# Performance work log

Measured on AMD Instinct MI355X. Metric: run time of the kernel, lower is better.

The kernel has to match this reference:

```python
import jax, jax.numpy as jnp
import numpy as np

H = 256; L = 4; NH = 8; S = 2; N = 1024; E = 32768


def _ln(x, g, b, eps=1e-5):
    m = x.mean(-1, keepdims=True)
    v = x.var(-1, keepdims=True)
    return (x - m) / jnp.sqrt(v + eps) * g + b


def _mha(h, in_w, in_b, out_w, out_b):
    # torch nn.MultiheadAttention (batch_first): h [B, T, H]
    B, T, Hd = h.shape
    qkv = h @ in_w.T + in_b  # [B, T, 3H]
    q, k, v = jnp.split(qkv, 3, axis=-1)
    d = Hd // NH
    def rs(a):
        return a.reshape(B, T, NH, d).transpose(0, 2, 1, 3)  # [B, nh, T, d]
    q, k, v = rs(q), rs(k), rs(v)
    att = jax.nn.softmax(jnp.einsum('bhqd,bhkd->bhqk', q, k) * (1.0 / np.sqrt(d)), axis=-1)
    o = jnp.einsum('bhqk,bhkd->bhqd', att, v).transpose(0, 2, 1, 3).reshape(B, T, Hd)
    return o @ out_w.T + out_b


def _forward(edge_index, x, fe_w1, fe_b1, fe_w2, fe_b2,
             g_inw, g_inb, g_outw, g_outb, g_m1w, g_m1b, g_m2w, g_m2b,
             g_n1g, g_n1b, g_n2g, g_n2b,
             t_inw, t_inb, t_outw, t_outb, t_l1w, t_l1b, t_l2w, t_l2b,
             t_n1g, t_n1b, t_n2g, t_n2b, o_w1, o_b1, o_w2, o_b2):
    row, col = edge_index[0], edge_index[1]
    # feature encoder: [S, N, 3] -> [S, N, H]
    h = jnp.maximum(x @ fe_w1.T + fe_b1, 0.0) @ fe_w2.T + fe_b2
    # construct_graph uses first 3 channels of encoded features as positions
    pos = h[..., :3]
    ea = pos[:, col] - pos[:, row]  # [S, E, 3] edge_attr, fixed across GNN layers
    cnt = jnp.maximum(jax.ops.segment_sum(jnp.ones((E,), h.dtype), row, num_segments=N), 1.0)
    for l in range(L):
        hn = _ln(h, g_n1g[l], g_n1b[l])
        a = _mha(hn, g_inw[l], g_inb[l], g_outw[l], g_outb[l]) + h  # dense attn over N nodes, S as batch
        ef = jnp.concatenate([a[:, col], ea], axis=-1)  # gather: [S, E, H+3]
        msg = jnp.maximum(ef @ g_m1w[l].T + g_m1b[l], 0.0) @ g_m2w[l].T + g_m2b[l]  # [S, E, H]
        agg = jax.vmap(lambda m: jax.ops.segment_sum(m, row, num_segments=N))(msg)  # scatter-sum
        agg = agg / cnt[None, :, None]  # scatter-mean
        h = _ln(agg, g_n2g[l], g_n2b[l]) + h
    # temporal transformer over S per node: [N, S, H] (B=1 so B*N = N)
    ht = h.transpose(1, 0, 2)
    for l in range(L):
        a = _mha(ht, t_inw[l], t_inb[l], t_outw[l], t_outb[l])
        ht = _ln(ht + a, t_n1g[l], t_n1b[l])  # post-norm TransformerEncoderLayer, relu FFN
        ff = jnp.maximum(ht @ t_l1w[l].T + t_l1b[l], 0.0) @ t_l2w[l].T + t_l2b[l]
        ht = _ln(ht + ff, t_n2g[l], t_n2b[l])
    last = ht[:, -1, :]  # [N, H]
    out = jnp.maximum(last @ o_w1.T + o_b1, 0.0) @ o_w2.T + o_b2  # [N, 3]
    # reshape(B,N,out_seq,-1).transpose(1,2).squeeze(0) with B=1, out_seq=1 -> [1, N, 3]
    return out.reshape(1, N, 3)


def setup_inputs():
    key = jax.random.key(0)
    ks = iter(jax.random.split(key, 40))
    def w(shape, s=0.02):
        return jax.random.normal(next(ks), shape, dtype=jnp.float32) * s
    inp = {}
    inp['x'] = jax.random.normal(next(ks), (S, N, 3), dtype=jnp.float32)
    inp['edge_index'] = jax.random.randint(next(ks), (2, E), 0, N, dtype=jnp.int32)
    inp['fe_w1'] = w((H, 3)); inp['fe_b1'] = jnp.zeros((H,), jnp.float32)
    inp['fe_w2'] = w((H, H)); inp['fe_b2'] = jnp.zeros((H,), jnp.float32)
    inp['g_inw'] = w((L, 3 * H, H)); inp['g_inb'] = jnp.zeros((L, 3 * H), jnp.float32)
    inp['g_outw'] = w((L, H, H)); inp['g_outb'] = jnp.zeros((L, H), jnp.float32)
    inp['g_m1w'] = w((L, H, H + 3)); inp['g_m1b'] = jnp.zeros((L, H), jnp.float32)
    inp['g_m2w'] = w((L, H, H)); inp['g_m2b'] = jnp.zeros((L, H), jnp.float32)
    inp['g_n1g'] = jnp.ones((L, H), jnp.float32); inp['g_n1b'] = jnp.zeros((L, H), jnp.float32)
    inp['g_n2g'] = jnp.ones((L, H), jnp.float32); inp['g_n2b'] = jnp.zeros((L, H), jnp.float32)
    inp['t_inw'] = w((L, 3 * H, H)); inp['t_inb'] = jnp.zeros((L, 3 * H), jnp.float32)
    inp['t_outw'] = w((L, H, H)); inp['t_outb'] = jnp.zeros((L, H), jnp.float32)
    inp['t_l1w'] = w((L, 4 * H, H)); inp['t_l1b'] = jnp.zeros((L, 4 * H), jnp.float32)
    inp['t_l2w'] = w((L, H, 4 * H)); inp['t_l2b'] = jnp.zeros((L, H), jnp.float32)
    inp['t_n1g'] = jnp.ones((L, H), jnp.float32); inp['t_n1b'] = jnp.zeros((L, H), jnp.float32)
    inp['t_n2g'] = jnp.ones((L, H), jnp.float32); inp['t_n2b'] = jnp.zeros((L, H), jnp.float32)
    inp['o_w1'] = w((H, H)); inp['o_b1'] = jnp.zeros((H,), jnp.float32)
    inp['o_w2'] = w((3, H)); inp['o_b2'] = jnp.zeros((3,), jnp.float32)
    return inp


def reference(x, edge_index, fe_w1, fe_b1, fe_w2, fe_b2,
              g_inw, g_inb, g_outw, g_outb, g_m1w, g_m1b, g_m2w, g_m2b,
              g_n1g, g_n1b, g_n2g, g_n2b,
              t_inw, t_inb, t_outw, t_outb, t_l1w, t_l1b, t_l2w, t_l2b,
              t_n1g, t_n1b, t_n2g, t_n2b, o_w1, o_b1, o_w2, o_b2):
    return _forward(edge_index, x, fe_w1, fe_b1, fe_w2, fe_b2,
                    g_inw, g_inb, g_outw, g_outb, g_m1w, g_m1b, g_m2w, g_m2b,
                    g_n1g, g_n1b, g_n2g, g_n2b,
                    t_inw, t_inb, t_outw, t_outb, t_l1w, t_l1b, t_l2w, t_l2b,
                    t_n1g, t_n1b, t_n2g, t_n2b, o_w1, o_b1, o_w2, o_b2)
```

## Files before the change

### kernel.cpp

```cpp
#include <hip/hip_runtime.h>
#include <math.h>

#define NN 1024
#define SS 2
#define HH 256
#define EE 32768
#define NHEAD 8
#define LL 4

template<bool RELU, bool RESID, bool ROWSCALE>
__global__ __launch_bounds__(256)
void gemm_xwt32(const float* __restrict__ X, int ldx,
                const float* __restrict__ W, int ldw,
                const float* __restrict__ bias,
                const float* __restrict__ resid, int ldr,
                const float* __restrict__ rowscale,
                float* __restrict__ Y, int ldy, int K)
{
    __shared__ __align__(16) float Xs[16][68];
    __shared__ __align__(16) float Ws[16][36];
    const int tid = threadIdx.x;
    const int bn0 = blockIdx.x * 32;
    const int bm0 = blockIdx.y * 64;
    const int tx = tid & 7, ty = tid >> 3;
    const int lc = tid & 15, lr = tid >> 4;
    float acc[2][4];
#pragma unroll
    for (int i = 0; i < 2; i++)
#pragma unroll
        for (int j = 0; j < 4; j++) acc[i][j] = 0.f;

    for (int k0 = 0; k0 < K; k0 += 16) {
#pragma unroll
        for (int i = 0; i < 4; i++) {
            int r = lr * 4 + i;
            Xs[lc][r] = X[(size_t)(bm0 + r) * ldx + k0 + lc];
        }
#pragma unroll
        for (int i = 0; i < 2; i++) {
            int r = lr * 2 + i;
            Ws[lc][r] = W[(size_t)(bn0 + r) * ldw + k0 + lc];
        }
        __syncthreads();
#pragma unroll
        for (int kk = 0; kk < 16; kk++) {
            float2 av = *reinterpret_cast<const float2*>(&Xs[kk][ty * 2]);
            float4 bv = *reinterpret_cast<const float4*>(&Ws[kk][tx * 4]);
            float a2[2] = {av.x, av.y};
            float b4[4] = {bv.x, bv.y, bv.z, bv.w};
#pragma unroll
            for (int i = 0; i < 2; i++)
#pragma unroll
                for (int j = 0; j < 4; j++)
                    acc[i][j] = fmaf(a2[i], b4[j], acc[i][j]);
        }
        __syncthreads();
    }
#pragma unroll
    for (int i = 0; i < 2; i++) {
        int m = bm0 + ty * 2 + i;
        float rs = ROWSCALE ? rowscale[m] : 1.f;
        float* yp = Y + (size_t)m * ldy + bn0 + tx * 4;
        const float* rp = RESID ? (resid + (size_t)m * ldr + bn0 + tx * 4) : nullptr;
#pragma unroll
        for (int j = 0; j < 4; j++) {
            float b = bias[bn0 + tx * 4 + j];
            float v = acc[i][j] + (ROWSCALE ? rs * b : b);
            if (RESID) v += rp[j];
            if (RELU) v = fmaxf(v, 0.f);
            yp[j] = v;
        }
    }
}

template<bool RESID>
__global__ __launch_bounds__(256)
void ln_kernel(const float* __restrict__ X, const float* __restrict__ g,
               const float* __restrict__ b, const float* __restrict__ resid,
               float* __restrict__ Y)
{
    int row = blockIdx.x, t = threadIdx.x;
    float v = X[(size_t)row * HH + t];
    float s1 = v, s2 = v * v;
#pragma unroll
    for (int m = 32; m >= 1; m >>= 1) {
        s1 += __shfl_xor(s1, m);
        s2 += __shfl_xor(s2, m);
    }
    __shared__ float w1[4], w2[4];
    if ((t & 63) == 0) { w1[t >> 6] = s1; w2[t >> 6] = s2; }
    __syncthreads();
    float tot1 = w1[0] + w1[1] + w1[2] + w1[3];
    float tot2 = w2[0] + w2[1] + w2[2] + w2[3];
    float mean = tot1 * (1.f / HH);
    float var = tot2 * (1.f / HH) - mean * mean;
    float inv = rsqrtf(var + 1e-5f);
    float out = (v - mean) * inv * g[t] + b[t];
    if (RESID) out += resid[(size_t)row * HH + t];
    Y[(size_t)row * HH + t] = out;
}

__global__ __launch_bounds__(256, 2)
void attn_graph_kernel(const float* __restrict__ qkv, float* __restrict__ out)
{
    const int s = blockIdx.z, hh = blockIdx.y, qt = blockIdx.x;
    const int tid = threadIdx.x;
    const int qslot = tid >> 4, sub = tid & 15;
    __shared__ __align__(16) float Qs[32][36];
    __shared__ __align__(16) float Ks[128][36];
    __shared__ __align__(16) float Vs[128][36];
    const float* base = qkv + (size_t)s * NN * 768;
    {
        int r = tid >> 3, c0 = (tid & 7) * 4;
        const float* src = base + (size_t)(qt * 32 + r) * 768 + hh * 32 + c0;
        *reinterpret_cast<float4*>(&Qs[r][c0]) = *reinterpret_cast<const float4*>(src);
    }
    __syncthreads();
    float qa[32], qb[32], oa[32], ob[32];
#pragma unroll
    for (int c = 0; c < 32; c++) {
        qa[c] = Qs[qslot * 2][c];
        qb[c] = Qs[qslot * 2 + 1][c];
        oa[c] = 0.f; ob[c] = 0.f;
    }
    float ma = -INFINITY, la = 0.f;
    float mb = -INFINITY, lb = 0.f;
    const float scale = 0.17677669529663687f;

    for (int kc = 0; kc < NN; kc += 128) {
        __syncthreads();
        {
            int r0 = tid >> 3, c0 = (tid & 7) * 4;
#pragma unroll
            for (int u = 0; u < 4; u++) {
                int r = r0 + 32 * u;
                const float* ksrc = base + (size_t)(kc + r) * 768 + 256 + hh * 32 + c0;
                *reinterpret_cast<float4*>(&Ks[r][c0]) = *reinterpret_cast<const float4*>(ksrc);
                *reinterpret_cast<float4*>(&Vs[r][c0]) = *reinterpret_cast<const float4*>(ksrc + 256);
            }
        }
        __syncthreads();
        float sa[8], sb[8];
#pragma unroll
        for (int i = 0; i < 8; i++) {
            int j = sub + 16 * i;
            float da = 0.f, db = 0.f;
#pragma unroll
            for (int c = 0; c < 32; c++) {
                float kv = Ks[j][c];
                da = fmaf(qa[c], kv, da);
                db = fmaf(qb[c], kv, db);
            }
            sa[i] = da * scale;
            sb[i] = db * scale;
        }
        float cma = sa[0], cmb = sb[0];
#pragma unroll
        for (int i = 1; i < 8; i++) { cma = fmaxf(cma, sa[i]); cmb = fmaxf(cmb, sb[i]); }
        float mna = fmaxf(ma, cma), mnb = fmaxf(mb, cmb);
        float ca = __expf(ma - mna), cb = __expf(mb - mnb);
        la *= ca; lb *= cb;
#pragma unroll
        for (int c = 0; c < 32; c++) { oa[c] *= ca; ob[c] *= cb; }
#pragma unroll
        for (int i = 0; i < 8; i++) {
            int j = sub + 16 * i;
            float pa = __expf(sa[i] - mna);
            float pb = __expf(sb[i] - mnb);
            la += pa; lb += pb;
#pragma unroll
            for (int c = 0; c < 32; c++) {
                float vv = Vs[j][c];
                oa[c] = fmaf(pa, vv, oa[c]);
                ob[c] = fmaf(pb, vv, ob[c]);
            }
        }
        ma = mna; mb = mnb;
    }
#pragma unroll
    for (int mask = 1; mask <= 8; mask <<= 1) {
        float m2a = __shfl_xor(ma, mask), l2a = __shfl_xor(la, mask);
        float mna = fmaxf(ma, m2a);
        float c1a = __expf(ma - mna), c2a = __expf(m2a - mna);
        la = la * c1a + l2a * c2a;
        float m2b = __shfl_xor(mb, mask), l2b = __shfl_xor(lb, mask);
        float mnb = fmaxf(mb, m2b);
        float c1b = __expf(mb - mnb), c2b = __expf(m2b - mnb);
        lb = lb * c1b + l2b * c2b;
#pragma unroll
        for (int c = 0; c < 32; c++) {
            float ta = __shfl_xor(oa[c], mask);
            oa[c] = oa[c] * c1a + ta * c2a;
            float tb = __shfl_xor(ob[c], mask);
            ob[c] = ob[c] * c1b + tb * c2b;
        }
        ma = mna; mb = mnb;
    }
    float ia = 1.f / la, ib = 1.f / lb;
    float* dA = out + ((size_t)s * NN + qt * 32 + qslot * 2) * HH + hh * 32;
    float* dB = dA + HH;
#pragma unroll
    for (int c2 = 0; c2 < 16; c2++) {
        if (c2 == sub) {
            *reinterpret_cast<float2*>(dA + c2 * 2) =
                make_float2(oa[c2 * 2] * ia, oa[c2 * 2 + 1] * ia);
            *reinterpret_cast<float2*>(dB + c2 * 2) =
                make_float2(ob[c2 * 2] * ib, ob[c2 * 2 + 1] * ib);
        }
    }
}

__global__ __launch_bounds__(256)
void attn_t2_kernel(const float* __restrict__ qkvt, float* __restrict__ out)
{
    int idx = blockIdx.x * 256 + threadIdx.x;
    int n = idx >> 3, hh = idx & 7;
    const float* p0 = qkvt + ((size_t)n * SS + 0) * 768 + hh * 32;
    const float* p1 = qkvt + ((size_t)n * SS + 1) * 768 + hh * 32;
    float s00 = 0, s01 = 0, s10 = 0, s11 = 0;
#pragma unroll
    for (int c4 = 0; c4 < 8; c4++) {
        float4 q0 = *reinterpret_cast<const float4*>(p0 + c4 * 4);
        float4 q1 = *reinterpret_cast<const float4*>(p1 + c4 * 4);
        float4 k0 = *reinterpret_cast<const float4*>(p0 + 256 + c4 * 4);
        float4 k1 = *reinterpret_cast<const float4*>(p1 + 256 + c4 * 4);
        s00 += q0.x * k0.x + q0.y * k0.y + q0.z * k0.z + q0.w * k0.w;
        s01 += q0.x * k1.x + q0.y * k1.y + q0.z * k1.z + q0.w * k1.w;
        s10 += q1.x * k0.x + q1.y * k0.y + q1.z * k0.z + q1.w * k0.w;
        s11 += q1.x * k1.x + q1.y * k1.y + q1.z * k1.z + q1.w * k1.w;
    }
    const float scale = 0.17677669529663687f;
    s00 *= scale; s01 *= scale; s10 *= scale; s11 *= scale;
    float m0 = fmaxf(s00, s01), m1 = fmaxf(s10, s11);
    float p00 = __expf(s00 - m0), p01 = __expf(s01 - m0);
    float p10 = __expf(s10 - m1), p11 = __expf(s11 - m1);
    float i0 = 1.f / (p00 + p01), i1 = 1.f / (p10 + p11);
    p00 *= i0; p01 *= i0; p10 *= i1; p11 *= i1;
    float* o0 = out + ((size_t)n * SS + 0) * HH + hh * 32;
    float* o1 = out + ((size_t)n * SS + 1) * HH + hh * 32;
#pragma unroll
    for (int c4 = 0; c4 < 8; c4++) {
        float4 v0 = *reinterpret_cast<const float4*>(p0 + 512 + c4 * 4);
        float4 v1 = *reinterpret_cast<const float4*>(p1 + 512 + c4 * 4);
        float4 r0, r1;
        r0.x = p00 * v0.x + p01 * v1.x; r0.y = p00 * v0.y + p01 * v1.y;
        r0.z = p00 * v0.z + p01 * v1.z; r0.w = p00 * v0.w + p01 * v1.w;
        r1.x = p10 * v0.x + p11 * v1.x; r1.y = p10 * v0.y + p11 * v1.y;
        r1.z = p10 * v0.z + p11 * v1.z; r1.w = p10 * v0.w + p11 * v1.w;
        *reinterpret_cast<float4*>(o0 + c4 * 4) = r0;
        *reinterpret_cast<float4*>(o1 + c4 * 4) = r1;
    }
}

__global__ __launch_bounds__(256)
void edge_agg_kernel(const float* __restrict__ P, const float* __restrict__ ea,
                     const float* __restrict__ W1,
                     const int* __restrict__ off, const int* __restrict__ eid,
                     const int* __restrict__ colIdx, const float* __restrict__ cnt,
                     float* __restrict__ Rn)
{
    const int n = blockIdx.x, s = blockIdx.y;
    const int t = threadIdx.x;
    const float w0 = W1[(size_t)t * 259 + 256];
    const float w1 = W1[(size_t)t * 259 + 257];
    const float w2 = W1[(size_t)t * 259 + 258];
    float acc = 0.f;
    const int beg = off[n], end = off[n + 1];
    const float* eab = ea + (size_t)s * EE * 3;
    const float* Pb = P + (size_t)s * NN * HH;
    for (int p = beg; p < end; ++p) {
        int e = eid[p];
        int c = colIdx[e];
        float e0 = eab[(size_t)e * 3 + 0];
        float e1 = eab[(size_t)e * 3 + 1];
        float e2 = eab[(size_t)e * 3 + 2];
        float u = Pb[(size_t)c * HH + t] + e0 * w0 + e1 * w1 + e2 * w2;
        acc += fmaxf(u, 0.f);
    }
    Rn[((size_t)s * NN + n) * HH + t] = acc / cnt[n];
}

__global__ __launch_bounds__(256)
void enc1_kernel(const float* __restrict__ x, const float* __restrict__ w1,
                 const float* __restrict__ b1, float* __restrict__ t0)
{
    int m = blockIdx.x, j = threadIdx.x;
    float x0 = x[(size_t)m * 3 + 0], x1 = x[(size_t)m * 3 + 1], x2 = x[(size_t)m * 3 + 2];
    float v = fmaf(x0, w1[j * 3 + 0], fmaf(x1, w1[j * 3 + 1], fmaf(x2, w1[j * 3 + 2], b1[j])));
    t0[(size_t)m * HH + j] = fmaxf(v, 0.f);
}

__global__ __launch_bounds__(256)
void deg_kernel(const int* __restrict__ rowIdx, int* __restrict__ deg)
{
    int e = blockIdx.x * 256 + threadIdx.x;
    atomicAdd(&deg[rowIdx[e]], 1);
}

__global__ __launch_bounds__(256)
void cnt_kernel(const int* __restrict__ deg, float* __restrict__ cnt,
                float* __restrict__ bscale)
{
    int n = blockIdx.x * 256 + threadIdx.x;
    int d = deg[n];
    cnt[n] = d > 0 ? (float)d : 1.f;
    float bs = d > 0 ? 1.f : 0.f;
    bscale[n] = bs;
    bscale[NN + n] = bs;
}

__global__ void scan1024(const int* __restrict__ deg, int* __restrict__ off)
{
    __shared__ int tmp[1024];
    int t = threadIdx.x;
    tmp[t] = deg[t];
    __syncthreads();
    for (int d = 1; d < 1024; d <<= 1) {
        int v = 0;
        if (t >= d) v = tmp[t - d];
        __syncthreads();
        if (t >= d) tmp[t] += v;
        __syncthreads();
    }
    off[t + 1] = tmp[t];
    if (t == 0) off[0] = 0;
}

__global__ __launch_bounds__(256)
void csr_scatter(const int* __restrict__ rowIdx, int* __restrict__ cursor,
                 int* __restrict__ eidb)
{
    int e = blockIdx.x * 256 + threadIdx.x;
    int p = atomicAdd(&cursor[rowIdx[e]], 1);
    eidb[p] = e;
}

__global__ __launch_bounds__(256)
void ea_kernel(const float* __restrict__ h, const int* __restrict__ rowIdx,
               const int* __restrict__ colIdx, float* __restrict__ ea)
{
    int idx = blockIdx.x * 256 + threadIdx.x;
    int e = idx & (EE - 1);
    int s = idx >> 15;
    int r = rowIdx[e], c = colIdx[e];
    const float* hb = h + (size_t)s * NN * HH;
    float* o = ea + (size_t)idx * 3;
    o[0] = hb[(size_t)c * HH + 0] - hb[(size_t)r * HH + 0];
    o[1] = hb[(size_t)c * HH + 1] - hb[(size_t)r * HH + 1];
    o[2] = hb[(size_t)c * HH + 2] - hb[(size_t)r * HH + 2];
}

__global__ __launch_bounds__(256)
void transpose_sn(const float* __restrict__ h, float* __restrict__ ht)
{
    int c = threadIdx.x, n = blockIdx.x, s = blockIdx.y;
    ht[((size_t)n * SS + s) * HH + c] = h[((size_t)s * NN + n) * HH + c];
}

__global__ __launch_bounds__(64)
void final_kernel(const float* __restrict__ o1, const float* __restrict__ w2,
                  const float* __restrict__ b2, float* __restrict__ out)
{
    int n = blockIdx.x, t = threadIdx.x;
    float a0 = 0, a1 = 0, a2 = 0;
#pragma unroll
    for (int r = 0; r < 4; r++) {
        float v = o1[(size_t)n * HH + t + 64 * r];
        a0 = fmaf(v, w2[0 * HH + t + 64 * r], a0);
        a1 = fmaf(v, w2[1 * HH + t + 64 * r], a1);
        a2 = fmaf(v, w2[2 * HH + t + 64 * r], a2);
    }
#pragma unroll
    for (int m = 32; m >= 1; m >>= 1) {
        a0 += __shfl_xor(a0, m);
        a1 += __shfl_xor(a1, m);
        a2 += __shfl_xor(a2, m);
    }
    if (t == 0) {
        out[(size_t)n * 3 + 0] = a0 + b2[0];
        out[(size_t)n * 3 + 1] = a1 + b2[1];
        out[(size_t)n * 3 + 2] = a2 + b2[2];
    }
}

extern "C" void kernel_launch(void* const* d_in, const int* in_sizes, int n_in,
                              void* d_out, int out_size, void* d_ws, size_t ws_size,
                              hipStream_t stream)
{
    const float* x      = (const float*)d_in[0];
    const int*   eidx   = (const int*)d_in[1];
    const float* fe_w1  = (const float*)d_in[2];
    const float* fe_b1  = (const float*)d_in[3];
    const float* fe_w2  = (const float*)d_in[4];
    const float* fe_b2  = (const float*)d_in[5];
    const float* g_inw  = (const float*)d_in[6];
    const float* g_inb  = (const float*)d_in[7];
    const float* g_outw = (const float*)d_in[8];
    const float* g_outb = (const float*)d_in[9];
    const float* g_m1w  = (const float*)d_in[10];
    const float* g_m1b  = (const float*)d_in[11];
    const float* g_m2w  = (const float*)d_in[12];
    const float* g_m2b  = (const float*)d_in[13];
    const float* g_n1g  = (const float*)d_in[14];
    const float* g_n1b  = (const float*)d_in[15];
    const float* g_n2g  = (const float*)d_in[16];
    const float* g_n2b  = (const float*)d_in[17];
    const float* t_inw  = (const float*)d_in[18];
    const float* t_inb  = (const float*)d_in[19];
    const float* t_outw = (const float*)d_in[20];
    const float* t_outb = (const float*)d_in[21];
    const float* t_l1w  = (const float*)d_in[22];
    const float* t_l1b  = (const float*)d_in[23];
    const float* t_l2w  = (const float*)d_in[24];
    const float* t_l2b  = (const float*)d_in[25];
    const float* t_n1g  = (const float*)d_in[26];
    const float* t_n1b  = (const float*)d_in[27];
    const float* t_n2g  = (const float*)d_in[28];
    const float* t_n2b  = (const float*)d_in[29];
    const float* o_w1   = (const float*)d_in[30];
    const float* o_b1   = (const float*)d_in[31];
    const float* o_w2   = (const float*)d_in[32];
    const float* o_b2   = (const float*)d_in[33];

    const int* rowIdx = eidx;
    const int* colIdx = eidx + EE;

    float* w = (float*)d_ws;
    const size_t F = (size_t)SS * NN * HH;
    float* h      = w;
    float* hn     = w + F;
    float* qkv    = w + 2 * F;
    float* attno  = w + 5 * F;
    float* a      = w + 6 * F;
    float* P      = w + 7 * F;
    float* Rn     = w + 8 * F;
    float* aggn   = w + 9 * F;
    float* ffh    = w + 10 * F;
    float* ea     = w + 14 * F;
    float* o1     = ea + (size_t)SS * EE * 3;
    float* cnt    = o1 + (size_t)NN * HH;
    float* bscale = cnt + NN;
    int* ib       = (int*)(bscale + 2 * NN);
    int* deg      = ib;
    int* off      = ib + NN;
    int* cursor   = ib + 2 * NN + 1;
    int* eidbuf   = ib + 3 * NN + 1;

    dim3 b256(256);

    float* t0 = qkv;
    enc1_kernel<<<dim3(SS * NN), b256, 0, stream>>>(x, fe_w1, fe_b1, t0);
    gemm_xwt32<false, false, false><<<dim3(8, 32), b256, 0, stream>>>(
        t0, HH, fe_w2, HH, fe_b2, nullptr, 0, nullptr, h, HH, HH);

    hipMemsetAsync(deg, 0, NN * sizeof(int), stream);
    deg_kernel<<<dim3(EE / 256), b256, 0, stream>>>(rowIdx, deg);
    cnt_kernel<<<dim3(NN / 256), b256, 0, stream>>>(deg, cnt, bscale);
    scan1024<<<dim3(1), dim3(1024), 0, stream>>>(deg, off);
    hipMemcpyAsync(cursor, off, NN * sizeof(int), hipMemcpyDeviceToDevice, stream);
    csr_scatter<<<dim3(EE / 256), b256, 0, stream>>>(rowIdx, cursor, eidbuf);
    ea_kernel<<<dim3(SS * EE / 256), b256, 0, stream>>>(h, rowIdx, colIdx, ea);

    for (int l = 0; l < LL; l++) {
        ln_kernel<false><<<dim3(SS * NN), b256, 0, stream>>>(
            h, g_n1g + l * HH, g_n1b + l * HH, nullptr, hn);
        gemm_xwt32<false, false, false><<<dim3(24, 32), b256, 0, stream>>>(
            hn, HH, g_inw + (size_t)l * 3 * HH * HH, HH, g_inb + l * 3 * HH,
            nullptr, 0, nullptr, qkv, 3 * HH, HH);
        attn_graph_kernel<<<dim3(32, NHEAD, SS), b256, 0, stream>>>(qkv, attno);
        gemm_xwt32<false, true, false><<<dim3(8, 32), b256, 0, stream>>>(
            attno, HH, g_outw + (size_t)l * HH * HH, HH, g_outb + l * HH,
            h, HH, nullptr, a, HH, HH);
        gemm_xwt32<false, false, false><<<dim3(8, 32), b256, 0, stream>>>(
            a, HH, g_m1w + (size_t)l * HH * 259, 259, g_m1b + l * HH,
            nullptr, 0, nullptr, P, HH, HH);
        edge_agg_kernel<<<dim3(NN, SS), b256, 0, stream>>>(
            P, ea, g_m1w + (size_t)l * HH * 259, off, eidbuf, colIdx, cnt, Rn);
        gemm_xwt32<false, false, true><<<dim3(8, 32), b256, 0, stream>>>(
            Rn, HH, g_m2w + (size_t)l * HH * HH, HH, g_m2b + l * HH,
            nullptr, 0, bscale, aggn, HH, HH);
        ln_kernel<true><<<dim3(SS * NN), b256, 0, stream>>>(
            aggn, g_n2g + l * HH, g_n2b + l * HH, h, h);
    }

    float* ht = hn;
    transpose_sn<<<dim3(NN, SS), b256, 0, stream>>>(h, ht);

    float* tmp = P;
    for (int l = 0; l < LL; l++) {
        gemm_xwt32<false, false, false><<<dim3(24, 32), b256, 0, stream>>>(
            ht, HH, t_inw + (size_t)l * 3 * HH * HH, HH, t_inb + l * 3 * HH,
            nullptr, 0, nullptr, qkv, 3 * HH, HH);
        attn_t2_kernel<<<dim3(NN * NHEAD / 256), b256, 0, stream>>>(qkv, attno);
        gemm_xwt32<false, true, false><<<dim3(8, 32), b256, 0, stream>>>(
            attno, HH, t_outw + (size_t)l * HH * HH, HH, t_outb + l * HH,
            ht, HH, nullptr, tmp, HH, HH);
        ln_kernel<false><<<dim3(SS * NN), b256, 0, stream>>>(
            tmp, t_n1g + l * HH, t_n1b + l * HH, nullptr, ht);
        gemm_xwt32<true, false, false><<<dim3(32, 32), b256, 0, stream>>>(
            ht, HH, t_l1w + (size_t)l * 4 * HH * HH, HH, t_l1b + l * 4 * HH,
            nullptr, 0, nullptr, ffh, 4 * HH, HH);
        gemm_xwt32<false, true, false><<<dim3(8, 32), b256, 0, stream>>>(
            ffh, 4 * HH, t_l2w + (size_t)l * HH * 4 * HH, 4 * HH, t_l2b + l * HH,
            ht, HH, nullptr, tmp, HH, 4 * HH);
        ln_kernel<false><<<dim3(SS * NN), b256, 0, stream>>>(
            tmp, t_n2g + l * HH, t_n2b + l * HH, nullptr, ht);
    }

    gemm_xwt32<true, false, false><<<dim3(8, 16), b256, 0, stream>>>(
        ht + HH, 2 * HH, o_w1, HH, o_b1, nullptr, 0, nullptr, o1, HH, HH);
    final_kernel<<<dim3(NN), dim3(64), 0, stream>>>(o1, o_w2, o_b2, (float*)d_out);
}
```

Measured before the change: 1.241 ms.

## Split-K GEMM across two thread halves; bf16 K/V in graph attention

The GEMM kernel now runs 512 threads per block. Each half accumulates one half of K into its own shared tiles, and the partial sums are reduced through shared memory before the epilogue. This is meant to add parallelism for the small grids these GEMMs launch. Separately, graph attention packs K/V tiles into bf16 in shared memory, halving LDS footprint and read traffic, and remaps block order, at the cost of precision loss in the attention scores and outputs.

```diff
diff --git a/kernel.cpp b/kernel.cpp
--- a/kernel.cpp
+++ b/kernel.cpp
@@ -8,8 +8,14 @@
 #define NHEAD 8
 #define LL 4
 
+__device__ inline unsigned int pk_bf16(float a, float b) {
+    unsigned int r;
+    asm volatile("v_cvt_pk_bf16_f32 %0, %1, %2" : "=v"(r) : "v"(a), "v"(b));
+    return r;
+}
+
 template<bool RELU, bool RESID, bool ROWSCALE>
-__global__ __launch_bounds__(256)
+__global__ __launch_bounds__(512)
 void gemm_xwt32(const float* __restrict__ X, int ldx,
                 const float* __restrict__ W, int ldw,
                 const float* __restrict__ bias,
@@ -17,35 +23,39 @@
                 const float* __restrict__ rowscale,
                 float* __restrict__ Y, int ldy, int K)
 {
-    __shared__ __align__(16) float Xs[16][68];
-    __shared__ __align__(16) float Ws[16][36];
-    const int tid = threadIdx.x;
+    __shared__ __align__(16) float Xs[2][16][68];
+    __shared__ __align__(16) float Ws[2][16][36];
+    __shared__ float accs[256][9];
+    const int tid = threadIdx.x & 255;
+    const int kh = threadIdx.x >> 8;
     const int bn0 = blockIdx.x * 32;
     const int bm0 = blockIdx.y * 64;
     const int tx = tid & 7, ty = tid >> 3;
     const int lc = tid & 15, lr = tid >> 4;
+    const int Kh = K >> 1;
+    const int kbase = kh * Kh;
     float acc[2][4];
 #pragma unroll
     for (int i = 0; i < 2; i++)
 #pragma unroll
         for (int j = 0; j < 4; j++) acc[i][j] = 0.f;
 
-    for (int k0 = 0; k0 < K; k0 += 16) {
+    for (int k0 = 0; k0 < Kh; k0 += 16) {
 #pragma unroll
         for (int i = 0; i < 4; i++) {
             int r = lr * 4 + i;
-            Xs[lc][r] = X[(size_t)(bm0 + r) * ldx + k0 + lc];
+            Xs[kh][lc][r] = X[(size_t)(bm0 + r) * ldx + kbase + k0 + lc];
         }
 #pragma unroll
         for (int i = 0; i < 2; i++) {
             int r = lr * 2 + i;
-            Ws[lc][r] = W[(size_t)(bn0 + r) * ldw + k0 + lc];
+            Ws[kh][lc][r] = W[(size_t)(bn0 + r) * ldw + kbase + k0 + lc];
         }
         __syncthreads();
 #pragma unroll
         for (int kk = 0; kk < 16; kk++) {
-            float2 av = *reinterpret_cast<const float2*>(&Xs[kk][ty * 2]);
-            float4 bv = *reinterpret_cast<const float4*>(&Ws[kk][tx * 4]);
+            float2 av = *reinterpret_cast<const float2*>(&Xs[kh][kk][ty * 2]);
+            float4 bv = *reinterpret_cast<const float4*>(&Ws[kh][kk][tx * 4]);
             float a2[2] = {av.x, av.y};
             float b4[4] = {bv.x, bv.y, bv.z, bv.w};
 #pragma unroll
@@ -56,19 +66,28 @@
         }
         __syncthreads();
     }
-#pragma unroll
-    for (int i = 0; i < 2; i++) {
-        int m = bm0 + ty * 2 + i;
-        float rs = ROWSCALE ? rowscale[m] : 1.f;
-        float* yp = Y + (size_t)m * ldy + bn0 + tx * 4;
-        const float* rp = RESID ? (resid + (size_t)m * ldr + bn0 + tx * 4) : nullptr;
-#pragma unroll
-        for (int j = 0; j < 4; j++) {
-            float b = bias[bn0 + tx * 4 + j];
-            float v = acc[i][j] + (ROWSCALE ? rs * b : b);
-            if (RESID) v += rp[j];
-            if (RELU) v = fmaxf(v, 0.f);
-            yp[j] = v;
+    if (kh == 1) {
+#pragma unroll
+        for (int i = 0; i < 2; i++)
+#pragma unroll
+            for (int j = 0; j < 4; j++) accs[tid][i * 4 + j] = acc[i][j];
+    }
+    __syncthreads();
+    if (kh == 0) {
+#pragma unroll
+        for (int i = 0; i < 2; i++) {
+            int m = bm0 + ty * 2 + i;
+            float rs = ROWSCALE ? rowscale[m] : 1.f;
+            float* yp = Y + (size_t)m * ldy + bn0 + tx * 4;
+            const float* rp = RESID ? (resid + (size_t)m * ldr + bn0 + tx * 4) : nullptr;
+#pragma unroll
+            for (int j = 0; j < 4; j++) {
+                float b = bias[bn0 + tx * 4 + j];
+                float v = acc[i][j] + accs[tid][i * 4 + j] + (ROWSCALE ? rs * b : b);
+                if (RESID) v += rp[j];
+                if (RELU) v = fmaxf(v, 0.f);
+                yp[j] = v;
+            }
         }
     }
 }
@@ -103,12 +122,14 @@
 __global__ __launch_bounds__(256, 2)
 void attn_graph_kernel(const float* __restrict__ qkv, float* __restrict__ out)
 {
-    const int s = blockIdx.z, hh = blockIdx.y, qt = blockIdx.x;
+    int flat = blockIdx.x + 32 * (blockIdx.y + 8 * blockIdx.z);
+    int nf = (flat & 7) * 64 + (flat >> 3);
+    const int qt = nf & 31, hh = (nf >> 5) & 7, s = nf >> 8;
     const int tid = threadIdx.x;
     const int qslot = tid >> 4, sub = tid & 15;
     __shared__ __align__(16) float Qs[32][36];
-    __shared__ __align__(16) float Ks[128][36];
-    __shared__ __align__(16) float Vs[128][36];
+    __shared__ __align__(16) unsigned int Ks[128][20];
+    __shared__ __align__(16) unsigned int Vs[128][20];
     const float* base = qkv + (size_t)s * NN * 768;
     {
         int r = tid >> 3, c0 = (tid & 7) * 4;
@@ -130,14 +151,35 @@
     for (int kc = 0; kc < NN; kc += 128) {
         __syncthreads();
         {
-            int r0 = tid >> 3, c0 = (tid & 7) * 4;
-#pragma unroll
-            for (int u = 0; u < 4; u++) {
-                int r = r0 + 32 * u;
-                const float* ksrc = base + (size_t)(kc + r) * 768 + 256 + hh * 32 + c0;
-                *reinterpret_cast<float4*>(&Ks[r][c0]) = *reinterpret_cast<const float4*>(ksrc);
-                *reinterpret_cast<float4*>(&Vs[r][c0]) = *reinterpret_cast<const float4*>(ksrc + 256);
+            int r = tid >> 1, ch0 = (tid & 1) * 16;
+            const float* ksrc = base + (size_t)(kc + r) * 768 + 256 + hh * 32 + ch0;
+            const float* vsrc = ksrc + 256;
+            uint4 kw0, kw1, vw0, vw1;
+            {
+                float4 f0 = *reinterpret_cast<const float4*>(ksrc);
+                float4 f1 = *reinterpret_cast<const float4*>(ksrc + 4);
+                float4 f2 = *reinterpret_cast<const float4*>(ksrc + 8);
+                float4 f3 = *reinterpret_cast<const float4*>(ksrc + 12);
+                kw0 = make_uint4(pk_bf16(f0.x, f0.y), pk_bf16(f0.z, f0.w),
+                                 pk_bf16(f1.x, f1.y), pk_bf16(f1.z, f1.w));
+                kw1 = make_uint4(pk_bf16(f2.x, f2.y), pk_bf16(f2.z, f2.w),
+                                 pk_bf16(f3.x, f3.y), pk_bf16(f3.z, f3.w));
             }
+            {
+                float4 f0 = *reinterpret_cast<const float4*>(vsrc);
+                float4 f1 = *reinterpret_cast<const float4*>(vsrc + 4);
+                float4 f2 = *reinterpret_cast<const float4*>(vsrc + 8);
+                float4 f3 = *reinterpret_cast<const float4*>(vsrc + 12);
+                vw0 = make_uint4(pk_bf16(f0.x, f0.y), pk_bf16(f0.z, f0.w),
+                                 pk_bf16(f1.x, f1.y), pk_bf16(f1.z, f1.w));
+                vw1 = make_uint4(pk_bf16(f2.x, f2.y), pk_bf16(f2.z, f2.w),
+                                 pk_bf16(f3.x, f3.y), pk_bf16(f3.z, f3.w));
+            }
+            int u0 = ch0 >> 1;
+            *reinterpret_cast<uint4*>(&Ks[r][u0])     = kw0;
+            *reinterpret_cast<uint4*>(&Ks[r][u0 + 4]) = kw1;
+            *reinterpret_cast<uint4*>(&Vs[r][u0])     = vw0;
+            *reinterpret_cast<uint4*>(&Vs[r][u0 + 4]) = vw1;
         }
         __syncthreads();
         float sa[8], sb[8];
@@ -145,11 +187,19 @@
         for (int i = 0; i < 8; i++) {
             int j = sub + 16 * i;
             float da = 0.f, db = 0.f;
-#pragma unroll
-            for (int c = 0; c < 32; c++) {
-                float kv = Ks[j][c];
-                da = fmaf(qa[c], kv, da);
-                db = fmaf(qb[c], kv, db);
+            const uint4* kp = reinterpret_cast<const uint4*>(&Ks[j][0]);
+#pragma unroll
+            for (int w4 = 0; w4 < 4; w4++) {
+                uint4 kw = kp[w4];
+                unsigned int uu[4] = {kw.x, kw.y, kw.z, kw.w};
+#pragma unroll
+                for (int p = 0; p < 4; p++) {
+                    int c = w4 * 8 + p * 2;
+                    float e0 = __uint_as_float(uu[p] << 16);
+                    float e1 = __uint_as_float(uu[p] & 0xFFFF0000u);
+                    da = fmaf(qa[c], e0, da); da = fmaf(qa[c + 1], e1, da);
+                    db = fmaf(qb[c], e0, db); db = fmaf(qb[c + 1], e1, db);
+                }
             }
             sa[i] = da * scale;
             sb[i] = db * scale;
@@ -168,11 +218,21 @@
             float pa = __expf(sa[i] - mna);
             float pb = __expf(sb[i] - mnb);
             la += pa; lb += pb;
-#pragma unroll
-            for (int c = 0; c < 32; c++) {
-                float vv = Vs[j][c];
-                oa[c] = fmaf(pa, vv, oa[c]);
-                ob[c] = fmaf(pb, vv, ob[c]);
+            const uint4* vp = reinterpret_cast<const uint4*>(&Vs[j][0]);
+#pragma unroll
+            for (int w4 = 0; w4 < 4; w4++) {
+                uint4 vw = vp[w4];
+                unsigned int uu[4] = {vw.x, vw.y, vw.z, vw.w};
+#pragma unroll
+                for (int p = 0; p < 4; p++) {
+                    int c = w4 * 8 + p * 2;
+                    float e0 = __uint_as_float(uu[p] << 16);
+                    float e1 = __uint_as_float(uu[p] & 0xFFFF0000u);
+                    oa[c]     = fmaf(pa, e0, oa[c]);
+                    oa[c + 1] = fmaf(pa, e1, oa[c + 1]);
+                    ob[c]     = fmaf(pb, e0, ob[c]);
+                    ob[c + 1] = fmaf(pb, e1, ob[c + 1]);
+                }
             }
         }
         ma = mna; mb = mnb;
@@ -447,10 +507,11 @@
     int* eidbuf   = ib + 3 * NN + 1;
 
     dim3 b256(256);
+    dim3 b512(512);
 
     float* t0 = qkv;
     enc1_kernel<<<dim3(SS * NN), b256, 0, stream>>>(x, fe_w1, fe_b1, t0);
-    gemm_xwt32<false, false, false><<<dim3(8, 32), b256, 0, stream>>>(
+    gemm_xwt32<false, false, false><<<dim3(8, 32), b512, 0, stream>>>(
         t0, HH, fe_w2, HH, fe_b2, nullptr, 0, nullptr, h, HH, HH);
 
     hipMemsetAsync(deg, 0, NN * sizeof(int), stream);
@@ -464,19 +525,19 @@
     for (int l = 0; l < LL; l++) {
         ln_kernel<false><<<dim3(SS * NN), b256, 0, stream>>>(
             h, g_n1g + l * HH, g_n1b + l * HH, nullptr, hn);
-        gemm_xwt32<false, false, false><<<dim3(24, 32), b256, 0, stream>>>(
+        gemm_xwt32<false, false, false><<<dim3(24, 32), b512, 0, stream>>>(
             hn, HH, g_inw + (size_t)l * 3 * HH * HH, HH, g_inb + l * 3 * HH,
             nullptr, 0, nullptr, qkv, 3 * HH, HH);
         attn_graph_kernel<<<dim3(32, NHEAD, SS), b256, 0, stream>>>(qkv, attno);
-        gemm_xwt32<false, true, false><<<dim3(8, 32), b256, 0, stream>>>(
+        gemm_xwt32<false, true, false><<<dim3(8, 32), b512, 0, stream>>>(
             attno, HH, g_outw + (size_t)l * HH * HH, HH, g_outb + l * HH,
             h, HH, nullptr, a, HH, HH);
-        gemm_xwt32<false, false, false><<<dim3(8, 32), b256, 0, stream>>>(
+        gemm_xwt32<false, false, false><<<dim3(8, 32), b512, 0, stream>>>(
             a, HH, g_m1w + (size_t)l * HH * 259, 259, g_m1b + l * HH,
             nullptr, 0, nullptr, P, HH, HH);
         edge_agg_kernel<<<dim3(NN, SS), b256, 0, stream>>>(
             P, ea, g_m1w + (size_t)l * HH * 259, off, eidbuf, colIdx, cnt, Rn);
-        gemm_xwt32<false, false, true><<<dim3(8, 32), b256, 0, stream>>>(
+        gemm_xwt32<false, false, true><<<dim3(8, 32), b512, 0, stream>>>(
             Rn, HH, g_m2w + (size_t)l * HH * HH, HH, g_m2b + l * HH,
             nullptr, 0, bscale, aggn, HH, HH);
         ln_kernel<true><<<dim3(SS * NN), b256, 0, stream>>>(
@@ -488,26 +549,26 @@
 
     float* tmp = P;
     for (int l = 0; l < LL; l++) {
-        gemm_xwt32<false, false, false><<<dim3(24, 32), b256, 0, stream>>>(
+        gemm_xwt32<false, false, false><<<dim3(24, 32), b512, 0, stream>>>(
             ht, HH, t_inw + (size_t)l * 3 * HH * HH, HH, t_inb + l * 3 * HH,
             nullptr, 0, nullptr, qkv, 3 * HH, HH);
         attn_t2_kernel<<<dim3(NN * NHEAD / 256), b256, 0, stream>>>(qkv, attno);
-        gemm_xwt32<false, true, false><<<dim3(8, 32), b256, 0, stream>>>(
+        gemm_xwt32<false, true, false><<<dim3(8, 32), b512, 0, stream>>>(
             attno, HH, t_outw + (size_t)l * HH * HH, HH, t_outb + l * HH,
             ht, HH, nullptr, tmp, HH, HH);
         ln_kernel<false><<<dim3(SS * NN), b256, 0, stream>>>(
             tmp, t_n1g + l * HH, t_n1b + l * HH, nullptr, ht);
-        gemm_xwt32<true, false, false><<<dim3(32, 32), b256, 0, stream>>>(
+        gemm_xwt32<true, false, false><<<dim3(32, 32), b512, 0, stream>>>(
             ht, HH, t_l1w + (size_t)l * 4 * HH * HH, HH, t_l1b + l * 4 * HH,
             nullptr, 0, nullptr, ffh, 4 * HH, HH);
-        gemm_xwt32<false, true, false><<<dim3(8, 32), b256, 0, stream>>>(
+        gemm_xwt32<false, true, false><<<dim3(8, 32), b512, 0, stream>>>(
             ffh, 4 * HH, t_l2w + (size_t)l * HH * 4 * HH, 4 * HH, t_l2b + l * HH,
             ht, HH, nullptr, tmp, HH, 4 * HH);
         ln_kernel<false><<<dim3(SS * NN), b256, 0, stream>>>(
             tmp, t_n2g + l * HH, t_n2b + l * HH, nullptr, ht);
     }
 
-    gemm_xwt32<true, false, false><<<dim3(8, 16), b256, 0, stream>>>(
+    gemm_xwt32<true, false, false><<<dim3(8, 16), b512, 0, stream>>>(
         ht + HH, 2 * HH, o_w1, HH, o_b1, nullptr, 0, nullptr, o1, HH, HH);
     final_kernel<<<dim3(NN), dim3(64), 0, stream>>>(o1, o_w2, o_b2, (float*)d_out);
 }
```

Result: slower. 1.733 ms (+39.6%).
